# Performance work log

Measured on AMD Instinct MI355X. Metric: run time of the kernel, lower is better.

The kernel has to match this reference:

```python
import jax, jax.numpy as jnp
import numpy as np

N, M, D, HEADS, LAYERS, STEPS = 1536, 768, 256, 8, 6, 100
S = N + M
DH = D // HEADS
VN_PER_CHECK = 6


def _build_code():
    rng = np.random.default_rng(0)
    H = np.zeros((M, N), np.float32)
    cols = rng.random((M, N)).argsort(1)[:, :VN_PER_CHECK]
    H[np.arange(M)[:, None], cols] = 1.0
    # Tanner-graph adjacency: self, cn<->vn edges, vn<->vn sharing a check
    A = np.eye(S, dtype=np.float32)
    A[N:, :N] += H
    A[:N, N:] += H.T
    A[:N, :N] += (H.T @ H > 0).astype(np.float32)
    mask = (A <= 0).astype(np.float32)  # 1 = attention disallowed
    return H, mask


def setup_inputs() -> dict:
    H, mask = _build_code()
    ks = jax.random.split(jax.random.key(0), 16)
    g = lambda i, shape, s=0.02: jax.random.normal(ks[i], shape, jnp.float32) * s
    return dict(
        r_t=jax.random.normal(ks[0], (N, 1), jnp.float32),
        H=jnp.asarray(H), mask=jnp.asarray(mask),
        src_embed=jax.random.uniform(ks[1], (1, S, D), dtype=jnp.float32),
        time_table=g(2, (STEPS, D), 1.0),
        Wq=g(3, (LAYERS, D, D)), Wk=g(4, (LAYERS, D, D)),
        Wv=g(5, (LAYERS, D, D)), Wo=g(6, (LAYERS, D, D)),
        W1=g(7, (LAYERS, D, 4 * D)), b1=jnp.zeros((LAYERS, 4 * D), jnp.float32),
        W2=g(8, (LAYERS, 4 * D, D)), b2=jnp.zeros((LAYERS, D), jnp.float32),
        ln1_g=jnp.ones((LAYERS, D), jnp.float32), ln1_b=jnp.zeros((LAYERS, D), jnp.float32),
        ln2_g=jnp.ones((LAYERS, D), jnp.float32), ln2_b=jnp.zeros((LAYERS, D), jnp.float32),
        fc_w=g(9, (D, 1)), fc_b=jnp.zeros((1,), jnp.float32),
        to_n_w=g(10, (1, 1)), to_n_b=jnp.zeros((1,), jnp.float32),
        t=17,
    )


def _ln(x, g, b):
    mu = x.mean(-1, keepdims=True)
    var = ((x - mu) ** 2).mean(-1, keepdims=True)
    return (x - mu) * jax.lax.rsqrt(var + 1e-6) * g + b


def _forward(r_t, H, mask, src_embed, time_table, Wq, Wk, Wv, Wo, W1, b1,
             W2, b2, ln1_g, ln1_b, ln2_g, ln2_b, fc_w, fc_b, to_n_w, to_n_b, t):
    bits = 0.5 * (1.0 - jnp.sign(r_t))                  # llr_to_bin, (N,1)
    synd = jnp.mod(H @ bits, 2.0)                       # syndrome, (M,1)
    nodes = jnp.concatenate([jnp.abs(r_t), synd], 0)    # (S,1)
    x = src_embed[0] * nodes * time_table[t][None, :]   # (S,D): node-scaled embeds * time embed
    neg = mask[None] * (-1e9)                           # additive Tanner-graph mask
    scale = 1.0 / np.sqrt(DH).astype(np.float32)
    for i in range(LAYERS):
        q = (x @ Wq[i]).reshape(S, HEADS, DH)
        k = (x @ Wk[i]).reshape(S, HEADS, DH)
        v = (x @ Wv[i]).reshape(S, HEADS, DH)
        scores = jnp.einsum('qhd,khd->hqk', q, k) * scale + neg  # (H,S,S)
        attn = jax.nn.softmax(scores, axis=-1)
        o = jnp.einsum('hqk,khd->qhd', attn, v).reshape(S, D) @ Wo[i]
        x = _ln(x + o, ln1_g[i], ln1_b[i])
        f = jax.nn.relu(x @ W1[i] + b1[i]) @ W2[i] + b2[i]
        x = _ln(x + f, ln2_g[i], ln2_b[i])
    logits = (x @ fc_w + fc_b)[:, 0]                    # fc: Dense(1), squeeze
    node_logits = logits[:N, None]                      # keep variable-node logits
    return node_logits @ to_n_w + to_n_b                # z_hat, (N,1)


def reference(r_t, H, mask, src_embed, time_table, Wq, Wk, Wv, Wo, W1, b1,
              W2, b2, ln1_g, ln1_b, ln2_g, ln2_b, fc_w, fc_b, to_n_w, to_n_b, t):
    return _forward(r_t, H, mask, src_embed, time_table, Wq, Wk, Wv, Wo, W1, b1,
                    W2, b2, ln1_g, ln1_b, ln2_g, ln2_b, fc_w, fc_b, to_n_w, to_n_b, t)
```

## Files before the change

### kernel.cpp

```cpp
#include <hip/hip_runtime.h>
#include <math.h>

#define N_  1536
#define M_  768
#define D_  256
#define HEADS_ 8
#define DH_ 32
#define LAYERS_ 6
#define S_  2304
#define SW_ (S_/32)
#define NSPLIT_ 4
#define SPLEN_ (S_/NSPLIT_)

typedef __attribute__((ext_vector_type(8))) short  s16x8;
typedef __attribute__((ext_vector_type(8))) __bf16 bf16x8;
typedef __attribute__((ext_vector_type(4))) float  f32x4;

static __device__ __forceinline__ f32x4 mfma16(s16x8 a, s16x8 b, f32x4 c) {
    return __builtin_amdgcn_mfma_f32_16x16x32_bf16(
        __builtin_bit_cast(bf16x8, a), __builtin_bit_cast(bf16x8, b), c, 0, 0, 0);
}

static __device__ __forceinline__ short f2bf(float f) {
    unsigned u = __builtin_bit_cast(unsigned, f);
    unsigned r = u + 0x7FFFu + ((u >> 16) & 1u);
    return (short)(r >> 16);
}
static __device__ __forceinline__ float bf2f(short s) {
    unsigned u = ((unsigned)(unsigned short)s) << 16;
    return __builtin_bit_cast(float, u);
}
static __device__ __forceinline__ void splitf(float f, short& h, short& l) {
    h = f2bf(f);
    l = f2bf(f - bf2f(h));
}


__global__ __launch_bounds__(256) void k_absr(const float* __restrict__ r, float* __restrict__ nodes) {
    int i = blockIdx.x * 256 + threadIdx.x;
    if (i < N_) nodes[i] = fabsf(r[i]);
}

__global__ __launch_bounds__(256) void k_synd(const float* __restrict__ r, const float* __restrict__ H,
                                              float* __restrict__ nodes) {
    int row = blockIdx.x;
    int tid = threadIdx.x;
    float s = 0.f;
    for (int j = tid; j < N_; j += 256) {
        float b = (r[j] < 0.f) ? 1.f : 0.f;
        s += H[row * N_ + j] * b;
    }
    for (int o = 32; o; o >>= 1) s += __shfl_down(s, o, 64);
    __shared__ float w4[4];
    if ((tid & 63) == 0) w4[tid >> 6] = s;
    __syncthreads();
    if (tid == 0) {
        float t = w4[0] + w4[1] + w4[2] + w4[3];
        nodes[N_ + row] = fmodf(t, 2.0f);
    }
}

__global__ __launch_bounds__(256) void k_maskpack(const float* __restrict__ mask, unsigned* __restrict__ bits) {
    int w = blockIdx.x * 256 + threadIdx.x;
    if (w >= S_ * SW_) return;
    int row = w / SW_, c0 = (w % SW_) * 32;
    unsigned b = 0;
    const float* mrow = mask + (size_t)row * S_ + c0;
    for (int j = 0; j < 32; ++j)
        if (mrow[j] != 0.f) b |= (1u << j);
    bits[w] = b;
}

__global__ __launch_bounds__(256) void k_embed(const float* __restrict__ src, const float* __restrict__ tt,
                                               const int* __restrict__ tptr, const float* __restrict__ nodes,
                                               float* __restrict__ x) {
    int s = blockIdx.x, d = threadIdx.x;
    int t = tptr[0];
    x[s * D_ + d] = src[s * D_ + d] * nodes[s] * tt[t * D_ + d];
}


__global__ __launch_bounds__(256) void k_wsplit(const float* __restrict__ W, short* __restrict__ oh,
                                                short* __restrict__ ol, int K, int NC,
                                                long in_ls, long out_ls) {
    __shared__ float T[32][33];
    int z = blockIdx.z;
    const float* Wz = W + (size_t)z * in_ls;
    short* ohz = oh + (size_t)z * out_ls;
    short* olz = ol + (size_t)z * out_ls;
    int n0 = blockIdx.x * 32, k0 = blockIdx.y * 32;
    int t = threadIdx.x;
    int r = t >> 3, c4 = (t & 7) * 4;
    float4 v = *(const float4*)(Wz + (size_t)(k0 + r) * NC + n0 + c4);
    T[r][c4 + 0] = v.x; T[r][c4 + 1] = v.y; T[r][c4 + 2] = v.z; T[r][c4 + 3] = v.w;
    __syncthreads();
    int n = t >> 3, k4 = (t & 7) * 4;
#pragma unroll
    for (int i = 0; i < 4; ++i) {
        float f = T[k4 + i][n];
        short hh, ll; splitf(f, hh, ll);
        ohz[(size_t)(n0 + n) * K + k0 + k4 + i] = hh;
        olz[(size_t)(n0 + n) * K + k0 + k4 + i] = ll;
    }
}


__global__ __launch_bounds__(256) void k_qksplit(const float* __restrict__ qkv, short* __restrict__ qkh,
                                                 short* __restrict__ qkl) {
    int u = (blockIdx.x * 256 + threadIdx.x) * 8;
    int s = u >> 9, c = u & 511;
    const float* p = qkv + (size_t)s * 768 + c;
    float4 a = *(const float4*)p, b = *(const float4*)(p + 4);
    float v[8] = {a.x, a.y, a.z, a.w, b.x, b.y, b.z, b.w};
    s16x8 vh, vl;
#pragma unroll
    for (int i = 0; i < 8; ++i) { short hh, ll; splitf(v[i], hh, ll); vh[i] = hh; vl[i] = ll; }
    *(s16x8*)(qkh + u) = vh;
    *(s16x8*)(qkl + u) = vl;
}

__global__ __launch_bounds__(256) void k_vsplit(const float* __restrict__ qkv, short* __restrict__ vth,
                                                short* __restrict__ vtl) {
    __shared__ short Th[32][72], Tl[32][72];
    int s0 = blockIdx.x * 64, h = blockIdx.y;
    int t = threadIdx.x;
    {
        int row = t >> 2, c8 = (t & 3) * 8;
        const float* p = qkv + (size_t)(s0 + row) * 768 + 512 + h * DH_ + c8;
        float4 a = *(const float4*)p, b = *(const float4*)(p + 4);
        float v[8] = {a.x, a.y, a.z, a.w, b.x, b.y, b.z, b.w};
#pragma unroll
        for (int i = 0; i < 8; ++i) { short hh, ll; splitf(v[i], hh, ll); Th[c8 + i][row] = hh; Tl[c8 + i][row] = ll; }
    }
    __syncthreads();
    {
        int dh = t >> 3, seg = (t & 7) * 8;
        *(s16x8*)(vth + (size_t)(h * DH_ + dh) * S_ + s0 + seg) = *(s16x8*)&Th[dh][seg];
        *(s16x8*)(vtl + (size_t)(h * DH_ + dh) * S_ + s0 + seg) = *(s16x8*)&Tl[dh][seg];
    }
}


__global__ __launch_bounds__(256) void k_mgemm(const float* __restrict__ A, const short* __restrict__ BTh,
                                               const short* __restrict__ BTl, float* __restrict__ C,
                                               int K, int NC, const float* __restrict__ bias, int relu) {
    __shared__ short Ah[32][72], Al[32][72];
    __shared__ short Bh[64][72], Bl[64][72];
    int tid = threadIdx.x;
    int w = tid >> 6, lane = tid & 63;
    int n0w = (w & 1) * 32, kh = w >> 1;
    int r0 = blockIdx.y * 32, c0 = blockIdx.x * 64;
    int g = lane >> 4, cl = lane & 15;

    f32x4 acc[2][2];
#pragma unroll
    for (int mt = 0; mt < 2; ++mt)
#pragma unroll
        for (int nt = 0; nt < 2; ++nt) acc[mt][nt] = (f32x4){0.f, 0.f, 0.f, 0.f};

    int arow = tid >> 3, akq = (tid & 7) * 8;
    int bn = tid >> 2, bkq = (tid & 3) * 16;

    for (int k0 = 0; k0 < K; k0 += 64) {
        __syncthreads();
        {
            const float* ap = A + (size_t)(r0 + arow) * K + k0 + akq;
            float4 a0 = *(const float4*)ap, a1 = *(const float4*)(ap + 4);
            float av[8] = {a0.x, a0.y, a0.z, a0.w, a1.x, a1.y, a1.z, a1.w};
            s16x8 vh, vl;
#pragma unroll
            for (int i = 0; i < 8; ++i) { short hh, ll; splitf(av[i], hh, ll); vh[i] = hh; vl[i] = ll; }
            *(s16x8*)&Ah[arow][akq] = vh;
            *(s16x8*)&Al[arow][akq] = vl;
        }
        {
            const short* bph = BTh + (size_t)(c0 + bn) * K + k0 + bkq;
            const short* bpl = BTl + (size_t)(c0 + bn) * K + k0 + bkq;
            *(s16x8*)&Bh[bn][bkq]     = *(const s16x8*)bph;
            *(s16x8*)&Bh[bn][bkq + 8] = *(const s16x8*)(bph + 8);
            *(s16x8*)&Bl[bn][bkq]     = *(const s16x8*)bpl;
            *(s16x8*)&Bl[bn][bkq + 8] = *(const s16x8*)(bpl + 8);
        }
        __syncthreads();
        int kb = kh * 32 + g * 8;
        s16x8 fAh0 = *(s16x8*)&Ah[cl][kb],      fAl0 = *(s16x8*)&Al[cl][kb];
        s16x8 fAh1 = *(s16x8*)&Ah[16 + cl][kb], fAl1 = *(s16x8*)&Al[16 + cl][kb];
        s16x8 fBh0 = *(s16x8*)&Bh[n0w + cl][kb],      fBl0 = *(s16x8*)&Bl[n0w + cl][kb];
        s16x8 fBh1 = *(s16x8*)&Bh[n0w + 16 + cl][kb], fBl1 = *(s16x8*)&Bl[n0w + 16 + cl][kb];
        acc[0][0] = mfma16(fAh0, fBh0, acc[0][0]);
        acc[0][0] = mfma16(fAl0, fBh0, acc[0][0]);
        acc[0][0] = mfma16(fAh0, fBl0, acc[0][0]);
        acc[0][1] = mfma16(fAh0, fBh1, acc[0][1]);
        acc[0][1] = mfma16(fAl0, fBh1, acc[0][1]);
        acc[0][1] = mfma16(fAh0, fBl1, acc[0][1]);
        acc[1][0] = mfma16(fAh1, fBh0, acc[1][0]);
        acc[1][0] = mfma16(fAl1, fBh0, acc[1][0]);
        acc[1][0] = mfma16(fAh1, fBl0, acc[1][0]);
        acc[1][1] = mfma16(fAh1, fBh1, acc[1][1]);
        acc[1][1] = mfma16(fAl1, fBh1, acc[1][1]);
        acc[1][1] = mfma16(fAh1, fBl1, acc[1][1]);
    }

    __syncthreads();
    float* red = (float*)&Bh[0][0];
    if (kh == 1) {
        float* rp = red + (w & 1) * 1024 + lane * 16;
#pragma unroll
        for (int mt = 0; mt < 2; ++mt)
#pragma unroll
            for (int nt = 0; nt < 2; ++nt)
#pragma unroll
                for (int r = 0; r < 4; ++r) rp[(mt * 2 + nt) * 4 + r] = acc[mt][nt][r];
    }
    __syncthreads();
    if (kh == 0) {
        const float* rp = red + (w & 1) * 1024 + lane * 16;
#pragma unroll
        for (int mt = 0; mt < 2; ++mt)
#pragma unroll
            for (int nt = 0; nt < 2; ++nt) {
                int col = c0 + n0w + nt * 16 + cl;
                float bb = bias ? bias[col] : 0.f;
#pragma unroll
                for (int r = 0; r < 4; ++r) {
                    float v = acc[mt][nt][r] + rp[(mt * 2 + nt) * 4 + r] + bb;
                    if (relu) v = fmaxf(v, 0.f);
                    C[(size_t)(r0 + mt * 16 + g * 4 + r) * NC + col] = v;
                }
            }
    }
}


__global__ __launch_bounds__(128) void k_attn(const short* __restrict__ qkh, const short* __restrict__ qkl,
                                              const short* __restrict__ vth, const short* __restrict__ vtl,
                                              const unsigned* __restrict__ mbits,
                                              float* __restrict__ po, float* __restrict__ pml) {
    __shared__ short Kh[64][40], Kl[64][40];
    __shared__ short Vh[32][72], Vl[32][72];
    __shared__ short Ph[32][72], Pl[32][72];
    __shared__ unsigned mwv[32][2];
    __shared__ float sfac[32];

    int h = blockIdx.x, q0 = blockIdx.y * 32, sp = blockIdx.z;
    int c_begin = sp * SPLEN_, c_end = c_begin + SPLEN_;
    int tid = threadIdx.x;
    int w = tid >> 6, lane = tid & 63;
    int g = lane >> 4, cl = lane & 15;
    int wq = w * 16;
    const float scale = 0.17677669529663687f;

    s16x8 fQh = *(const s16x8*)(qkh + (size_t)(q0 + wq + cl) * 512 + h * DH_ + g * 8);
    s16x8 fQl = *(const s16x8*)(qkl + (size_t)(q0 + wq + cl) * 512 + h * DH_ + g * 8);

    int krow = tid & 63, kb0 = (tid >> 6) * 16;
    int vdh = tid >> 2, vb0 = (tid & 3) * 16;
    s16x8 rKh0, rKh1, rKl0, rKl1, rVh0, rVh1, rVl0, rVl1;
    {
        const short* ph = qkh + (size_t)(c_begin + krow) * 512 + 256 + h * DH_ + kb0;
        const short* pl = qkl + (size_t)(c_begin + krow) * 512 + 256 + h * DH_ + kb0;
        rKh0 = *(const s16x8*)ph; rKh1 = *(const s16x8*)(ph + 8);
        rKl0 = *(const s16x8*)pl; rKl1 = *(const s16x8*)(pl + 8);
        const short* vh = vth + (size_t)(h * DH_ + vdh) * S_ + c_begin + vb0;
        const short* vl = vtl + (size_t)(h * DH_ + vdh) * S_ + c_begin + vb0;
        rVh0 = *(const s16x8*)vh; rVh1 = *(const s16x8*)(vh + 8);
        rVl0 = *(const s16x8*)vl; rVl1 = *(const s16x8*)(vl + 8);
    }

    float m = -3.0e38f, l = 0.f;
    f32x4 accO[2] = {(f32x4){0.f,0.f,0.f,0.f}, (f32x4){0.f,0.f,0.f,0.f}};

    for (int c0 = c_begin; c0 < c_end; c0 += 64) {
        __syncthreads();
        {
            *(s16x8*)&Kh[krow][kb0]     = rKh0;
            *(s16x8*)&Kh[krow][kb0 + 8] = rKh1;
            *(s16x8*)&Kl[krow][kb0]     = rKl0;
            *(s16x8*)&Kl[krow][kb0 + 8] = rKl1;
            *(s16x8*)&Vh[vdh][vb0]      = rVh0;
            *(s16x8*)&Vh[vdh][vb0 + 8]  = rVh1;
            *(s16x8*)&Vl[vdh][vb0]      = rVl0;
            *(s16x8*)&Vl[vdh][vb0 + 8]  = rVl1;
        }
        if (tid < 64) mwv[tid >> 1][tid & 1] = mbits[(size_t)(q0 + (tid >> 1)) * SW_ + (c0 >> 5) + (tid & 1)];
        if (c0 + 64 < c_end) {
            const short* ph = qkh + (size_t)(c0 + 64 + krow) * 512 + 256 + h * DH_ + kb0;
            const short* pl = qkl + (size_t)(c0 + 64 + krow) * 512 + 256 + h * DH_ + kb0;
            rKh0 = *(const s16x8*)ph; rKh1 = *(const s16x8*)(ph + 8);
            rKl0 = *(const s16x8*)pl; rKl1 = *(const s16x8*)(pl + 8);
            const short* vh = vth + (size_t)(h * DH_ + vdh) * S_ + c0 + 64 + vb0;
            const short* vl = vtl + (size_t)(h * DH_ + vdh) * S_ + c0 + 64 + vb0;
            rVh0 = *(const s16x8*)vh; rVh1 = *(const s16x8*)(vh + 8);
            rVl0 = *(const s16x8*)vl; rVl1 = *(const s16x8*)(vl + 8);
        }
        __syncthreads();

        unsigned mw0 = mwv[wq + cl][0], mw1 = mwv[wq + cl][1];

        f32x4 sc[4];
#pragma unroll
        for (int nt2 = 0; nt2 < 4; ++nt2) {
            s16x8 fKh = *(s16x8*)&Kh[nt2 * 16 + cl][g * 8], fKl = *(s16x8*)&Kl[nt2 * 16 + cl][g * 8];
            f32x4 z = (f32x4){0.f, 0.f, 0.f, 0.f};
            z = mfma16(fKh, fQh, z);
            z = mfma16(fKl, fQh, z);
            z = mfma16(fKh, fQl, z);
            sc[nt2] = z;
        }

        float sv[4][4];
#pragma unroll
        for (int nt2 = 0; nt2 < 4; ++nt2) {
            unsigned wsel = (nt2 & 2) ? mw1 : mw0;
#pragma unroll
            for (int r = 0; r < 4; ++r) {
                int bitpos = ((nt2 & 1) << 4) + (g << 2) + r;
                sv[nt2][r] = ((wsel >> bitpos) & 1u) ? -1.0e30f : sc[nt2][r] * scale;
            }
        }

        float tmax = sv[0][0];
#pragma unroll
        for (int nt2 = 0; nt2 < 4; ++nt2)
#pragma unroll
            for (int r = 0; r < 4; ++r) tmax = fmaxf(tmax, sv[nt2][r]);
        tmax = fmaxf(tmax, __shfl_xor(tmax, 16));
        tmax = fmaxf(tmax, __shfl_xor(tmax, 32));
        float mn = fmaxf(m, tmax);
        float sf = __expf(m - mn);
        m = mn;
        float psum = 0.f;
#pragma unroll
        for (int nt2 = 0; nt2 < 4; ++nt2)
#pragma unroll
            for (int r = 0; r < 4; ++r) {
                float p = __expf(sv[nt2][r] - mn);
                psum += p;
                short ph = f2bf(p);
                Ph[wq + cl][nt2 * 16 + (g << 2) + r] = ph;
                Pl[wq + cl][nt2 * 16 + (g << 2) + r] = f2bf(p - bf2f(ph));
            }
        psum += __shfl_xor(psum, 16);
        psum += __shfl_xor(psum, 32);
        l = l * sf + psum;

        if (g == 0) sfac[wq + cl] = sf;
        float4 sf4 = *(float4*)&sfac[wq + (g << 2)];
#pragma unroll
        for (int nt = 0; nt < 2; ++nt) {
            accO[nt][0] *= sf4.x; accO[nt][1] *= sf4.y;
            accO[nt][2] *= sf4.z; accO[nt][3] *= sf4.w;
        }

#pragma unroll
        for (int kc = 0; kc < 2; ++kc) {
            s16x8 fPh = *(s16x8*)&Ph[wq + cl][kc * 32 + g * 8];
            s16x8 fPl = *(s16x8*)&Pl[wq + cl][kc * 32 + g * 8];
#pragma unroll
            for (int nt = 0; nt < 2; ++nt) {
                s16x8 fVh = *(s16x8*)&Vh[nt * 16 + cl][kc * 32 + g * 8];
                s16x8 fVl = *(s16x8*)&Vl[nt * 16 + cl][kc * 32 + g * 8];
                accO[nt] = mfma16(fPh, fVh, accO[nt]);
                accO[nt] = mfma16(fPl, fVh, accO[nt]);
                accO[nt] = mfma16(fPh, fVl, accO[nt]);
            }
        }
    }

#pragma unroll
    for (int nt = 0; nt < 2; ++nt)
#pragma unroll
        for (int r = 0; r < 4; ++r) {
            int row = q0 + wq + g * 4 + r;
            po[((size_t)sp * S_ + row) * D_ + h * DH_ + nt * 16 + cl] = accO[nt][r];
        }
    if (g == 0) {
        int row = q0 + wq + cl;
        size_t base = (((size_t)sp * S_ + row) * HEADS_ + h) * 2;
        pml[base] = m;
        pml[base + 1] = l;
    }
}


__global__ __launch_bounds__(256) void k_acomb(const float* __restrict__ po, const float* __restrict__ pml,
                                               float* __restrict__ o) {
    int row = blockIdx.x, d = threadIdx.x, h = d >> 5;
    float m[NSPLIT_], l[NSPLIT_];
#pragma unroll
    for (int sp = 0; sp < NSPLIT_; ++sp) {
        size_t base = (((size_t)sp * S_ + row) * HEADS_ + h) * 2;
        m[sp] = pml[base];
        l[sp] = pml[base + 1];
    }
    float M = fmaxf(fmaxf(m[0], m[1]), fmaxf(m[2], m[3]));
    float L = 0.f, acc = 0.f;
#pragma unroll
    for (int sp = 0; sp < NSPLIT_; ++sp) {
        float wgt = __expf(m[sp] - M);
        L += l[sp] * wgt;
        acc += po[((size_t)sp * S_ + row) * D_ + d] * wgt;
    }
    o[(size_t)row * D_ + d] = acc / L;
}


__global__ __launch_bounds__(256) void k_addln(float* __restrict__ x, const float* __restrict__ add,
                                               const float* __restrict__ gg, const float* __restrict__ bb) {
    int row = blockIdx.x, d = threadIdx.x;
    float val = x[row * D_ + d] + add[row * D_ + d];

    __shared__ float w4[4];
    __shared__ float bc[2];

    float ss = val;
    for (int o = 32; o; o >>= 1) ss += __shfl_down(ss, o, 64);
    if ((d & 63) == 0) w4[d >> 6] = ss;
    __syncthreads();
    if (d == 0) bc[0] = (w4[0] + w4[1] + w4[2] + w4[3]) * (1.f / D_);
    __syncthreads();
    float mu = bc[0];
    float c = val - mu;
    float vs = c * c;
    for (int o = 32; o; o >>= 1) vs += __shfl_down(vs, o, 64);
    __syncthreads();
    if ((d & 63) == 0) w4[d >> 6] = vs;
    __syncthreads();
    if (d == 0) bc[1] = (w4[0] + w4[1] + w4[2] + w4[3]) * (1.f / D_);
    __syncthreads();
    float var = bc[1];
    float rr = rsqrtf(var + 1e-6f);
    x[row * D_ + d] = c * rr * gg[d] + bb[d];
}


__global__ __launch_bounds__(256) void k_final(const float* __restrict__ x, const float* __restrict__ fcw,
                                               const float* __restrict__ fcb, const float* __restrict__ tnw,
                                               const float* __restrict__ tnb, float* __restrict__ out) {
    int row = blockIdx.x, d = threadIdx.x;
    float p = x[row * D_ + d] * fcw[d];
    for (int o = 32; o; o >>= 1) p += __shfl_down(p, o, 64);
    __shared__ float w4[4];
    if ((d & 63) == 0) w4[d >> 6] = p;
    __syncthreads();
    if (d == 0) {
        float s = w4[0] + w4[1] + w4[2] + w4[3];
        out[row] = (s + fcb[0]) * tnw[0] + tnb[0];
    }
}


extern "C" void kernel_launch(void* const* d_in, const int* in_sizes, int n_in,
                              void* d_out, int out_size, void* d_ws, size_t ws_size,
                              hipStream_t stream) {
    const float* r_t   = (const float*)d_in[0];
    const float* H     = (const float*)d_in[1];
    const float* mask  = (const float*)d_in[2];
    const float* src   = (const float*)d_in[3];
    const float* tt    = (const float*)d_in[4];
    const float* Wq    = (const float*)d_in[5];
    const float* Wk    = (const float*)d_in[6];
    const float* Wv    = (const float*)d_in[7];
    const float* Wo    = (const float*)d_in[8];
    const float* W1    = (const float*)d_in[9];
    const float* b1    = (const float*)d_in[10];
    const float* W2    = (const float*)d_in[11];
    const float* b2    = (const float*)d_in[12];
    const float* ln1g  = (const float*)d_in[13];
    const float* ln1b  = (const float*)d_in[14];
    const float* ln2g  = (const float*)d_in[15];
    const float* ln2b  = (const float*)d_in[16];
    const float* fcw   = (const float*)d_in[17];
    const float* fcb   = (const float*)d_in[18];
    const float* tnw   = (const float*)d_in[19];
    const float* tnb   = (const float*)d_in[20];
    const int*   tptr  = (const int*)d_in[21];
    float* out = (float*)d_out;

    float* ws    = (float*)d_ws;
    float* x     = ws;
    float* qkv   = x    + S_ * D_;
    float* ao    = qkv  + S_ * 768;
    float* tmp   = ao   + S_ * D_;
    float* h1    = tmp  + S_ * D_;
    float* nodes = h1   + S_ * 4 * D_;
    unsigned* mbits = (unsigned*)(nodes + S_);
    short* WqkvTh = (short*)(mbits + S_ * SW_);
    short* WqkvTl = WqkvTh + LAYERS_ * 768 * 256;
    short* WoTh   = WqkvTl + LAYERS_ * 768 * 256;
    short* WoTl   = WoTh   + LAYERS_ * 256 * 256;
    short* W1Th   = WoTl   + LAYERS_ * 256 * 256;
    short* W1Tl   = W1Th   + LAYERS_ * 1024 * 256;
    short* W2Th   = W1Tl   + LAYERS_ * 1024 * 256;
    short* W2Tl   = W2Th   + LAYERS_ * 256 * 1024;
    short* qkh    = W2Tl   + LAYERS_ * 256 * 1024;
    short* qkl    = qkh    + S_ * 512;
    short* vth    = qkl    + S_ * 512;
    short* vtl    = vth    + 256 * S_;
    float* po     = (float*)(vtl + 256 * S_);
    float* pml    = po + (size_t)NSPLIT_ * S_ * D_;

    k_absr<<<(N_ + 255) / 256, 256, 0, stream>>>(r_t, nodes);
    k_synd<<<M_, 256, 0, stream>>>(r_t, H, nodes);
    k_maskpack<<<(S_ * SW_ + 255) / 256, 256, 0, stream>>>(mask, mbits);
    k_embed<<<S_, 256, 0, stream>>>(src, tt, tptr, nodes, x);

    k_wsplit<<<dim3(8, 8, 6),  256, 0, stream>>>(Wq, WqkvTh,             WqkvTl,             256, 256,  65536, 196608);
    k_wsplit<<<dim3(8, 8, 6),  256, 0, stream>>>(Wk, WqkvTh + 256 * 256, WqkvTl + 256 * 256, 256, 256,  65536, 196608);
    k_wsplit<<<dim3(8, 8, 6),  256, 0, stream>>>(Wv, WqkvTh + 512 * 256, WqkvTl + 512 * 256, 256, 256,  65536, 196608);
    k_wsplit<<<dim3(8, 8, 6),  256, 0, stream>>>(Wo, WoTh, WoTl, 256, 256,  65536, 65536);
    k_wsplit<<<dim3(32, 8, 6), 256, 0, stream>>>(W1, W1Th, W1Tl, 256, 1024, 262144, 262144);
    k_wsplit<<<dim3(8, 32, 6), 256, 0, stream>>>(W2, W2Th, W2Tl, 1024, 256, 262144, 262144);

    for (int i = 0; i < LAYERS_; ++i) {
        k_mgemm<<<dim3(12, 72), 256, 0, stream>>>(x, WqkvTh + (size_t)i * 196608, WqkvTl + (size_t)i * 196608,
                                                  qkv, 256, 768, nullptr, 0);
        k_qksplit<<<576, 256, 0, stream>>>(qkv, qkh, qkl);
        k_vsplit<<<dim3(36, 8), 256, 0, stream>>>(qkv, vth, vtl);
        k_attn<<<dim3(HEADS_, S_ / 32, NSPLIT_), 128, 0, stream>>>(qkh, qkl, vth, vtl, mbits, po, pml);
        k_acomb<<<S_, 256, 0, stream>>>(po, pml, ao);
        k_mgemm<<<dim3(4, 72), 256, 0, stream>>>(ao, WoTh + (size_t)i * 65536, WoTl + (size_t)i * 65536,
                                                 tmp, 256, 256, nullptr, 0);
        k_addln<<<S_, 256, 0, stream>>>(x, tmp, ln1g + i * D_, ln1b + i * D_);
        k_mgemm<<<dim3(16, 72), 256, 0, stream>>>(x, W1Th + (size_t)i * 262144, W1Tl + (size_t)i * 262144,
                                                  h1, 256, 1024, b1 + i * 4 * D_, 1);
        k_mgemm<<<dim3(4, 72), 256, 0, stream>>>(h1, W2Th + (size_t)i * 262144, W2Tl + (size_t)i * 262144,
                                                 tmp, 1024, 256, b2 + i * D_, 0);
        k_addln<<<S_, 256, 0, stream>>>(x, tmp, ln2g + i * D_, ln2b + i * D_);
    }

    k_final<<<N_, 256, 0, stream>>>(x, fcw, fcb, tnw, tnb, out);
}
```

Baseline: 801.8 us.

## Produce bf16 hi/lo split activations in producer epilogues, drop qksplit kernel

Moves the fp32-to-bf16 hi/lo splitting of activations out of the GEMM A-tile load and into the kernels that produce them (embed, add+layernorm, attention combine, GEMM epilogues). The QKV GEMM now writes split halves directly, so the separate q/k split kernel is removed and attention and v-transpose read the split buffers in place. This is meant to remove redundant split work, which was repeated across column blocks, plus one launch per layer. In exchange, producers write two short arrays, and the GEMM epilogue does scalar short stores.

```diff
diff --git a/kernel.cpp b/kernel.cpp
--- a/kernel.cpp
+++ b/kernel.cpp
@@ -73,10 +73,15 @@
 
 __global__ __launch_bounds__(256) void k_embed(const float* __restrict__ src, const float* __restrict__ tt,
                                                const int* __restrict__ tptr, const float* __restrict__ nodes,
-                                               float* __restrict__ x) {
+                                               float* __restrict__ x, short* __restrict__ xh,
+                                               short* __restrict__ xl) {
     int s = blockIdx.x, d = threadIdx.x;
     int t = tptr[0];
-    x[s * D_ + d] = src[s * D_ + d] * nodes[s] * tt[t * D_ + d];
+    float v = src[s * D_ + d] * nodes[s] * tt[t * D_ + d];
+    x[s * D_ + d] = v;
+    short hh, ll; splitf(v, hh, ll);
+    xh[s * D_ + d] = hh;
+    xl[s * D_ + d] = ll;
 }
 
 
@@ -104,33 +109,17 @@
     }
 }
 
-
-__global__ __launch_bounds__(256) void k_qksplit(const float* __restrict__ qkv, short* __restrict__ qkh,
-                                                 short* __restrict__ qkl) {
-    int u = (blockIdx.x * 256 + threadIdx.x) * 8;
-    int s = u >> 9, c = u & 511;
-    const float* p = qkv + (size_t)s * 768 + c;
-    float4 a = *(const float4*)p, b = *(const float4*)(p + 4);
-    float v[8] = {a.x, a.y, a.z, a.w, b.x, b.y, b.z, b.w};
-    s16x8 vh, vl;
-#pragma unroll
-    for (int i = 0; i < 8; ++i) { short hh, ll; splitf(v[i], hh, ll); vh[i] = hh; vl[i] = ll; }
-    *(s16x8*)(qkh + u) = vh;
-    *(s16x8*)(qkl + u) = vl;
-}
-
-__global__ __launch_bounds__(256) void k_vsplit(const float* __restrict__ qkv, short* __restrict__ vth,
-                                                short* __restrict__ vtl) {
+__global__ __launch_bounds__(256) void k_vsplit(const short* __restrict__ qkvh, const short* __restrict__ qkvl,
+                                                short* __restrict__ vth, short* __restrict__ vtl) {
     __shared__ short Th[32][72], Tl[32][72];
     int s0 = blockIdx.x * 64, h = blockIdx.y;
     int t = threadIdx.x;
     {
         int row = t >> 2, c8 = (t & 3) * 8;
-        const float* p = qkv + (size_t)(s0 + row) * 768 + 512 + h * DH_ + c8;
-        float4 a = *(const float4*)p, b = *(const float4*)(p + 4);
-        float v[8] = {a.x, a.y, a.z, a.w, b.x, b.y, b.z, b.w};
-#pragma unroll
-        for (int i = 0; i < 8; ++i) { short hh, ll; splitf(v[i], hh, ll); Th[c8 + i][row] = hh; Tl[c8 + i][row] = ll; }
+        s16x8 a = *(const s16x8*)(qkvh + (size_t)(s0 + row) * 768 + 512 + h * DH_ + c8);
+        s16x8 b = *(const s16x8*)(qkvl + (size_t)(s0 + row) * 768 + 512 + h * DH_ + c8);
+#pragma unroll
+        for (int i = 0; i < 8; ++i) { Th[c8 + i][row] = a[i]; Tl[c8 + i][row] = b[i]; }
     }
     __syncthreads();
     {
@@ -141,9 +130,11 @@
 }
 
 
-__global__ __launch_bounds__(256) void k_mgemm(const float* __restrict__ A, const short* __restrict__ BTh,
-                                               const short* __restrict__ BTl, float* __restrict__ C,
-                                               int K, int NC, const float* __restrict__ bias, int relu) {
+__global__ __launch_bounds__(256) void k_mgemm(const short* __restrict__ Ah_in, const short* __restrict__ Al_in,
+                                               const short* __restrict__ BTh, const short* __restrict__ BTl,
+                                               float* __restrict__ Cf, short* __restrict__ Ch,
+                                               short* __restrict__ Cl, int K, int NC,
+                                               const float* __restrict__ bias, int relu) {
     __shared__ short Ah[32][72], Al[32][72];
     __shared__ short Bh[64][72], Bl[64][72];
     int tid = threadIdx.x;
@@ -164,14 +155,8 @@
     for (int k0 = 0; k0 < K; k0 += 64) {
         __syncthreads();
         {
-            const float* ap = A + (size_t)(r0 + arow) * K + k0 + akq;
-            float4 a0 = *(const float4*)ap, a1 = *(const float4*)(ap + 4);
-            float av[8] = {a0.x, a0.y, a0.z, a0.w, a1.x, a1.y, a1.z, a1.w};
-            s16x8 vh, vl;
-#pragma unroll
-            for (int i = 0; i < 8; ++i) { short hh, ll; splitf(av[i], hh, ll); vh[i] = hh; vl[i] = ll; }
-            *(s16x8*)&Ah[arow][akq] = vh;
-            *(s16x8*)&Al[arow][akq] = vl;
+            *(s16x8*)&Ah[arow][akq] = *(const s16x8*)(Ah_in + (size_t)(r0 + arow) * K + k0 + akq);
+            *(s16x8*)&Al[arow][akq] = *(const s16x8*)(Al_in + (size_t)(r0 + arow) * K + k0 + akq);
         }
         {
             const short* bph = BTh + (size_t)(c0 + bn) * K + k0 + bkq;
@@ -225,14 +210,20 @@
                 for (int r = 0; r < 4; ++r) {
                     float v = acc[mt][nt][r] + rp[(mt * 2 + nt) * 4 + r] + bb;
                     if (relu) v = fmaxf(v, 0.f);
-                    C[(size_t)(r0 + mt * 16 + g * 4 + r) * NC + col] = v;
+                    size_t idx = (size_t)(r0 + mt * 16 + g * 4 + r) * NC + col;
+                    if (Ch) {
+                        short hh, ll; splitf(v, hh, ll);
+                        Ch[idx] = hh; Cl[idx] = ll;
+                    } else {
+                        Cf[idx] = v;
+                    }
                 }
             }
     }
 }
 
 
-__global__ __launch_bounds__(128) void k_attn(const short* __restrict__ qkh, const short* __restrict__ qkl,
+__global__ __launch_bounds__(128) void k_attn(const short* __restrict__ qkvh, const short* __restrict__ qkvl,
                                               const short* __restrict__ vth, const short* __restrict__ vtl,
                                               const unsigned* __restrict__ mbits,
                                               float* __restrict__ po, float* __restrict__ pml) {
@@ -250,15 +241,15 @@
     int wq = w * 16;
     const float scale = 0.17677669529663687f;
 
-    s16x8 fQh = *(const s16x8*)(qkh + (size_t)(q0 + wq + cl) * 512 + h * DH_ + g * 8);
-    s16x8 fQl = *(const s16x8*)(qkl + (size_t)(q0 + wq + cl) * 512 + h * DH_ + g * 8);
+    s16x8 fQh = *(const s16x8*)(qkvh + (size_t)(q0 + wq + cl) * 768 + h * DH_ + g * 8);
+    s16x8 fQl = *(const s16x8*)(qkvl + (size_t)(q0 + wq + cl) * 768 + h * DH_ + g * 8);
 
     int krow = tid & 63, kb0 = (tid >> 6) * 16;
     int vdh = tid >> 2, vb0 = (tid & 3) * 16;
     s16x8 rKh0, rKh1, rKl0, rKl1, rVh0, rVh1, rVl0, rVl1;
     {
-        const short* ph = qkh + (size_t)(c_begin + krow) * 512 + 256 + h * DH_ + kb0;
-        const short* pl = qkl + (size_t)(c_begin + krow) * 512 + 256 + h * DH_ + kb0;
+        const short* ph = qkvh + (size_t)(c_begin + krow) * 768 + 256 + h * DH_ + kb0;
+        const short* pl = qkvl + (size_t)(c_begin + krow) * 768 + 256 + h * DH_ + kb0;
         rKh0 = *(const s16x8*)ph; rKh1 = *(const s16x8*)(ph + 8);
         rKl0 = *(const s16x8*)pl; rKl1 = *(const s16x8*)(pl + 8);
         const short* vh = vth + (size_t)(h * DH_ + vdh) * S_ + c_begin + vb0;
@@ -284,8 +275,8 @@
         }
         if (tid < 64) mwv[tid >> 1][tid & 1] = mbits[(size_t)(q0 + (tid >> 1)) * SW_ + (c0 >> 5) + (tid & 1)];
         if (c0 + 64 < c_end) {
-            const short* ph = qkh + (size_t)(c0 + 64 + krow) * 512 + 256 + h * DH_ + kb0;
-            const short* pl = qkl + (size_t)(c0 + 64 + krow) * 512 + 256 + h * DH_ + kb0;
+            const short* ph = qkvh + (size_t)(c0 + 64 + krow) * 768 + 256 + h * DH_ + kb0;
+            const short* pl = qkvl + (size_t)(c0 + 64 + krow) * 768 + 256 + h * DH_ + kb0;
             rKh0 = *(const s16x8*)ph; rKh1 = *(const s16x8*)(ph + 8);
             rKl0 = *(const s16x8*)pl; rKl1 = *(const s16x8*)(pl + 8);
             const short* vh = vth + (size_t)(h * DH_ + vdh) * S_ + c0 + 64 + vb0;
@@ -384,7 +375,7 @@
 
 
 __global__ __launch_bounds__(256) void k_acomb(const float* __restrict__ po, const float* __restrict__ pml,
-                                               float* __restrict__ o) {
+                                               short* __restrict__ aoh, short* __restrict__ aol) {
     int row = blockIdx.x, d = threadIdx.x, h = d >> 5;
     float m[NSPLIT_], l[NSPLIT_];
 #pragma unroll
@@ -401,12 +392,16 @@
         L += l[sp] * wgt;
         acc += po[((size_t)sp * S_ + row) * D_ + d] * wgt;
     }
-    o[(size_t)row * D_ + d] = acc / L;
+    float v = acc / L;
+    short hh, ll; splitf(v, hh, ll);
+    aoh[(size_t)row * D_ + d] = hh;
+    aol[(size_t)row * D_ + d] = ll;
 }
 
 
 __global__ __launch_bounds__(256) void k_addln(float* __restrict__ x, const float* __restrict__ add,
-                                               const float* __restrict__ gg, const float* __restrict__ bb) {
+                                               const float* __restrict__ gg, const float* __restrict__ bb,
+                                               short* __restrict__ xh, short* __restrict__ xl) {
     int row = blockIdx.x, d = threadIdx.x;
     float val = x[row * D_ + d] + add[row * D_ + d];
 
@@ -430,7 +425,11 @@
     __syncthreads();
     float var = bc[1];
     float rr = rsqrtf(var + 1e-6f);
-    x[row * D_ + d] = c * rr * gg[d] + bb[d];
+    float out = c * rr * gg[d] + bb[d];
+    x[row * D_ + d] = out;
+    short hh, ll; splitf(out, hh, ll);
+    xh[row * D_ + d] = hh;
+    xl[row * D_ + d] = ll;
 }
 
 
@@ -479,31 +478,34 @@
 
     float* ws    = (float*)d_ws;
     float* x     = ws;
-    float* qkv   = x    + S_ * D_;
-    float* ao    = qkv  + S_ * 768;
-    float* tmp   = ao   + S_ * D_;
-    float* h1    = tmp  + S_ * D_;
-    float* nodes = h1   + S_ * 4 * D_;
+    float* tmp   = x    + S_ * D_;
+    float* po    = tmp  + S_ * D_;
+    float* pml   = po   + (size_t)NSPLIT_ * S_ * D_;
+    float* nodes = pml  + (size_t)NSPLIT_ * S_ * HEADS_ * 2;
     unsigned* mbits = (unsigned*)(nodes + S_);
     short* WqkvTh = (short*)(mbits + S_ * SW_);
-    short* WqkvTl = WqkvTh + LAYERS_ * 768 * 256;
-    short* WoTh   = WqkvTl + LAYERS_ * 768 * 256;
-    short* WoTl   = WoTh   + LAYERS_ * 256 * 256;
-    short* W1Th   = WoTl   + LAYERS_ * 256 * 256;
-    short* W1Tl   = W1Th   + LAYERS_ * 1024 * 256;
-    short* W2Th   = W1Tl   + LAYERS_ * 1024 * 256;
-    short* W2Tl   = W2Th   + LAYERS_ * 256 * 1024;
-    short* qkh    = W2Tl   + LAYERS_ * 256 * 1024;
-    short* qkl    = qkh    + S_ * 512;
-    short* vth    = qkl    + S_ * 512;
-    short* vtl    = vth    + 256 * S_;
-    float* po     = (float*)(vtl + 256 * S_);
-    float* pml    = po + (size_t)NSPLIT_ * S_ * D_;
+    short* WqkvTl = WqkvTh + (size_t)LAYERS_ * 768 * 256;
+    short* WoTh   = WqkvTl + (size_t)LAYERS_ * 768 * 256;
+    short* WoTl   = WoTh   + (size_t)LAYERS_ * 256 * 256;
+    short* W1Th   = WoTl   + (size_t)LAYERS_ * 256 * 256;
+    short* W1Tl   = W1Th   + (size_t)LAYERS_ * 1024 * 256;
+    short* W2Th   = W1Tl   + (size_t)LAYERS_ * 1024 * 256;
+    short* W2Tl   = W2Th   + (size_t)LAYERS_ * 256 * 1024;
+    short* xh     = W2Tl   + (size_t)LAYERS_ * 256 * 1024;
+    short* xl     = xh  + (size_t)S_ * 256;
+    short* qkvh   = xl  + (size_t)S_ * 256;
+    short* qkvl   = qkvh + (size_t)S_ * 768;
+    short* vth    = qkvl + (size_t)S_ * 768;
+    short* vtl    = vth + (size_t)256 * S_;
+    short* aoh    = vtl + (size_t)256 * S_;
+    short* aol    = aoh + (size_t)S_ * 256;
+    short* h1h    = aol + (size_t)S_ * 256;
+    short* h1l    = h1h + (size_t)S_ * 1024;
 
     k_absr<<<(N_ + 255) / 256, 256, 0, stream>>>(r_t, nodes);
     k_synd<<<M_, 256, 0, stream>>>(r_t, H, nodes);
     k_maskpack<<<(S_ * SW_ + 255) / 256, 256, 0, stream>>>(mask, mbits);
-    k_embed<<<S_, 256, 0, stream>>>(src, tt, tptr, nodes, x);
+    k_embed<<<S_, 256, 0, stream>>>(src, tt, tptr, nodes, x, xh, xl);
 
     k_wsplit<<<dim3(8, 8, 6),  256, 0, stream>>>(Wq, WqkvTh,             WqkvTl,             256, 256,  65536, 196608);
     k_wsplit<<<dim3(8, 8, 6),  256, 0, stream>>>(Wk, WqkvTh + 256 * 256, WqkvTl + 256 * 256, 256, 256,  65536, 196608);
@@ -513,20 +515,19 @@
     k_wsplit<<<dim3(8, 32, 6), 256, 0, stream>>>(W2, W2Th, W2Tl, 1024, 256, 262144, 262144);
 
     for (int i = 0; i < LAYERS_; ++i) {
-        k_mgemm<<<dim3(12, 72), 256, 0, stream>>>(x, WqkvTh + (size_t)i * 196608, WqkvTl + (size_t)i * 196608,
-                                                  qkv, 256, 768, nullptr, 0);
-        k_qksplit<<<576, 256, 0, stream>>>(qkv, qkh, qkl);
-        k_vsplit<<<dim3(36, 8), 256, 0, stream>>>(qkv, vth, vtl);
-        k_attn<<<dim3(HEADS_, S_ / 32, NSPLIT_), 128, 0, stream>>>(qkh, qkl, vth, vtl, mbits, po, pml);
-        k_acomb<<<S_, 256, 0, stream>>>(po, pml, ao);
-        k_mgemm<<<dim3(4, 72), 256, 0, stream>>>(ao, WoTh + (size_t)i * 65536, WoTl + (size_t)i * 65536,
-                                                 tmp, 256, 256, nullptr, 0);
-        k_addln<<<S_, 256, 0, stream>>>(x, tmp, ln1g + i * D_, ln1b + i * D_);
-        k_mgemm<<<dim3(16, 72), 256, 0, stream>>>(x, W1Th + (size_t)i * 262144, W1Tl + (size_t)i * 262144,
-                                                  h1, 256, 1024, b1 + i * 4 * D_, 1);
-        k_mgemm<<<dim3(4, 72), 256, 0, stream>>>(h1, W2Th + (size_t)i * 262144, W2Tl + (size_t)i * 262144,
-                                                 tmp, 1024, 256, b2 + i * D_, 0);
-        k_addln<<<S_, 256, 0, stream>>>(x, tmp, ln2g + i * D_, ln2b + i * D_);
+        k_mgemm<<<dim3(12, 72), 256, 0, stream>>>(xh, xl, WqkvTh + (size_t)i * 196608, WqkvTl + (size_t)i * 196608,
+                                                  nullptr, qkvh, qkvl, 256, 768, nullptr, 0);
+        k_vsplit<<<dim3(36, 8), 256, 0, stream>>>(qkvh, qkvl, vth, vtl);
+        k_attn<<<dim3(HEADS_, S_ / 32, NSPLIT_), 128, 0, stream>>>(qkvh, qkvl, vth, vtl, mbits, po, pml);
+        k_acomb<<<S_, 256, 0, stream>>>(po, pml, aoh, aol);
+        k_mgemm<<<dim3(4, 72), 256, 0, stream>>>(aoh, aol, WoTh + (size_t)i * 65536, WoTl + (size_t)i * 65536,
+                                                 tmp, nullptr, nullptr, 256, 256, nullptr, 0);
+        k_addln<<<S_, 256, 0, stream>>>(x, tmp, ln1g + i * D_, ln1b + i * D_, xh, xl);
+        k_mgemm<<<dim3(16, 72), 256, 0, stream>>>(xh, xl, W1Th + (size_t)i * 262144, W1Tl + (size_t)i * 262144,
+                                                  nullptr, h1h, h1l, 256, 1024, b1 + i * 4 * D_, 1);
+        k_mgemm<<<dim3(4, 72), 256, 0, stream>>>(h1h, h1l, W2Th + (size_t)i * 262144, W2Tl + (size_t)i * 262144,
+                                                 tmp, nullptr, nullptr, 1024, 256, b2 + i * D_, 0);
+        k_addln<<<S_, 256, 0, stream>>>(x, tmp, ln2g + i * D_, ln2b + i * D_, xh, xl);
     }
 
     k_final<<<N_, 256, 0, stream>>>(x, fcw, fcb, tnw, tnb, out);
```

After: 811.2 us. Within noise of the previous version (+1.2%).
